# Performance work log

Hardware: AMD Instinct MI355X
Metric: run time of the kernel (lower is better)

Reference implementation:

```python
import jax, jax.numpy as jnp
import numpy as np

L, D, H, P = 4096, 512, 512, 16  # seq_len, feature_dim, attention_hidden_dim, padding_size


def setup_inputs() -> dict:
    key = jax.random.key(0)
    k1, k2, k3, k4 = jax.random.split(key, 4)
    x = jax.random.normal(k1, (L, D), dtype=jnp.float32)
    s = 1.0 / np.sqrt(D).astype(np.float32)
    Ww = jax.random.uniform(k2, (H, D), jnp.float32, -s, s)   # nn.Linear(D, H, bias=False).weight
    Wu = jax.random.uniform(k3, (H, D), jnp.float32, -s, s)
    sv = 1.0 / np.sqrt(H).astype(np.float32)
    Wv = jax.random.uniform(k4, (1, H), jnp.float32, -sv, sv)  # nn.Linear(H, 1, bias=False).weight
    return {"x": x, "Ww": Ww, "Wu": Wu, "Wv": Wv}


def _window_gather(x):
    # zero-pad P rows on each end of the sequence, then for each position i
    # gather the 2P neighbors (P left, P right), excluding the center.
    xp = jnp.pad(x, ((P, P), (0, 0)))
    off = jnp.concatenate([jnp.arange(P), jnp.arange(P + 1, 2 * P + 1)])  # [2P]
    idx = jnp.arange(x.shape[0])[:, None] + off[None, :]                  # [L, 2P]
    return xp[idx]                                                        # [L, 2P, D]


def reference(x, Ww, Wu, Wv):
    x_local = _window_gather(x)                                  # [L, 2P, D]
    wx = x @ Ww.T                                                # [L, H] (center, computed once vs torch repeat)
    ux = jnp.einsum('lwd,hd->lwh', x_local, Wu)                  # [L, 2P, H]
    energy = jnp.tanh(wx[:, None, :] + ux)                       # [L, 2P, H]
    scores = jnp.einsum('lwh,h->lw', energy, Wv[0])              # [L, 2P]
    attn = jax.nn.softmax(scores, axis=1)                        # softmax over window
    g = jnp.einsum('lw,lwd->ld', attn, x_local)                  # [L, D]
    return g
```

## Files before the change

### kernel.cpp

```cpp
#include <hip/hip_runtime.h>

#define L_SEQ 4096
#define D_DIM 512
#define H_DIM 512
#define P_PAD 16
#define LB 4
#define LOG2E2 2.885390081777927f
#define LOG2E  1.4426950408889634f

typedef __bf16 bf16x8 __attribute__((ext_vector_type(8)));
typedef float  f32x4  __attribute__((ext_vector_type(4)));

extern "C" __device__ float __ocml_native_exp2_f32(float);

__device__ __forceinline__ float exp2_fast(float x) {
#if __has_builtin(__builtin_amdgcn_exp2f)
    return __builtin_amdgcn_exp2f(x);
#else
    return __ocml_native_exp2_f32(x);
#endif
}

__device__ __forceinline__ ushort f2bf(float f) {
    unsigned u = __float_as_uint(f);
    return (ushort)((u + 0x7FFFu + ((u >> 16) & 1u)) >> 16);
}

__global__ __launch_bounds__(256) void convert_kernel(
    const float* __restrict__ x, const float* __restrict__ Ww,
    const float* __restrict__ Wu, ushort* __restrict__ xb,
    ushort* __restrict__ Wwb, ushort* __restrict__ Wub)
{
    int i = blockIdx.x * 256 + threadIdx.x;
    const float* src; ushort* dst; int off;
    if (i < 524288)      { src = x;  dst = xb;  off = i; }
    else if (i < 589824) { src = Ww; dst = Wwb; off = i - 524288; }
    else                 { src = Wu; dst = Wub; off = i - 589824; }
    float4 v = ((const float4*)src)[off];
    ushort4 o;
    o.x = f2bf(v.x); o.y = f2bf(v.y); o.z = f2bf(v.z); o.w = f2bf(v.w);
    ((ushort4*)dst)[off] = o;
}

__global__ __launch_bounds__(256, 2) void dual_gemm_mfma(
    const ushort* __restrict__ xb, const ushort* __restrict__ Wwb,
    const ushort* __restrict__ Wub, float* __restrict__ Ew, float* __restrict__ Eu)
{
    const ushort* Bm = blockIdx.z ? Wub : Wwb;
    float*       out = blockIdx.z ? Eu : Ew;
    const int m0 = blockIdx.x * 128;
    const int n0 = blockIdx.y * 64;

    __shared__ __align__(16) ushort As[2][128 * 64];
    __shared__ __align__(16) ushort Bs[2][64 * 64];

    const int tid  = threadIdx.x;
    const int wv   = tid >> 6;
    const int lane = tid & 63;
    const int wm   = (wv >> 1) * 64;
    const int wn   = (wv & 1) * 32;
    const int lr   = lane & 15;
    const int lg   = lane >> 4;
    const int rx   = lr & 7;

    f32x4 acc[4][2] = {};

    auto stage = [&](int t, int buf) {
        const int k0 = t * 64;
        #pragma unroll
        for (int i = 0; i < 4; ++i) {
            int c = i * 256 + tid;
            int row = c >> 3, q = c & 7;
            const ushort* src = xb + (size_t)(m0 + row) * D_DIM + k0 + ((q ^ (row & 7)) * 8);
            ushort* dst = &As[buf][(i * 256 + wv * 64) * 8];
            __builtin_amdgcn_global_load_lds(
                (const __attribute__((address_space(1))) void*)src,
                (__attribute__((address_space(3))) void*)dst, 16, 0, 0);
        }
        #pragma unroll
        for (int i = 0; i < 2; ++i) {
            int c = i * 256 + tid;
            int row = c >> 3, q = c & 7;
            const ushort* src = Bm + (size_t)(n0 + row) * D_DIM + k0 + ((q ^ (row & 7)) * 8);
            ushort* dst = &Bs[buf][(i * 256 + wv * 64) * 8];
            __builtin_amdgcn_global_load_lds(
                (const __attribute__((address_space(1))) void*)src,
                (__attribute__((address_space(3))) void*)dst, 16, 0, 0);
        }
    };

    auto compute = [&](int buf) {
        #pragma unroll
        for (int kk = 0; kk < 2; ++kk) {
            bf16x8 a[4], b[2];
            #pragma unroll
            for (int mi = 0; mi < 4; ++mi)
                a[mi] = *(const bf16x8*)&As[buf][(wm + mi * 16 + lr) * 64 +
                                                 (((kk * 4 + lg) ^ rx) * 8)];
            #pragma unroll
            for (int ni = 0; ni < 2; ++ni)
                b[ni] = *(const bf16x8*)&Bs[buf][(wn + ni * 16 + lr) * 64 +
                                                 (((kk * 4 + lg) ^ rx) * 8)];
            #pragma unroll
            for (int mi = 0; mi < 4; ++mi)
                #pragma unroll
                for (int ni = 0; ni < 2; ++ni)
                    acc[mi][ni] = __builtin_amdgcn_mfma_f32_16x16x32_bf16(
                        a[mi], b[ni], acc[mi][ni], 0, 0, 0);
        }
    };

    stage(0, 0);
    __syncthreads();
    #pragma unroll
    for (int t = 0; t < 7; ++t) {
        stage(t + 1, (t + 1) & 1);
        compute(t & 1);
        __syncthreads();
    }
    compute(1);

    #pragma unroll
    for (int mi = 0; mi < 4; ++mi)
        #pragma unroll
        for (int ni = 0; ni < 2; ++ni)
            #pragma unroll
            for (int r = 0; r < 4; ++r)
                out[(size_t)(m0 + wm + mi * 16 + lg * 4 + r) * H_DIM + n0 + wn + ni * 16 + lr] =
                    exp2_fast(LOG2E2 * acc[mi][ni][r]);
}

template<bool EDGE>
__device__ __forceinline__ float score_phase(
    const float* __restrict__ Eu, int l, int lane,
    const float* ewr, const float* wvn)
{
    const float* base = Eu + (size_t)l * H_DIM + lane * 8;
    float sc = 0.0f;
    #pragma unroll
    for (int wg = 0; wg < 8; ++wg) {
        f32x4 u[4][2];
        #pragma unroll
        for (int wi = 0; wi < 4; ++wi) {
            const int w = wg * 4 + wi;
            const int j = (w < P_PAD) ? (w - P_PAD) : (w - P_PAD + 1);
            const float* p;
            if (EDGE) {
                int n = l + j;
                n = min(max(n, 0), L_SEQ - 1);
                p = Eu + (size_t)n * H_DIM + lane * 8;
            } else {
                p = base + j * H_DIM;
            }
            u[wi][0] = ((const f32x4*)p)[0];
            u[wi][1] = ((const f32x4*)p)[1];
        }
        float a4[4];
        #pragma unroll
        for (int wi = 0; wi < 4; ++wi) {
            float a = 0.0f;
            #pragma unroll
            for (int e = 0; e < 8; ++e) {
                float eu = u[wi][e >> 2][e & 3];
                float q  = __builtin_fmaf(ewr[e], eu, 1.0f);
                a = __builtin_fmaf(wvn[e], __builtin_amdgcn_rcpf(q), a);
            }
            a4[wi] = a;
        }
        const bool b0 = lane & 1, b1 = lane & 2;
        float s01 = b0 ? a4[0] : a4[1];
        float r01 = __shfl_xor(s01, 1);
        float c0  = (b0 ? a4[1] : a4[0]) + r01;
        float s23 = b0 ? a4[2] : a4[3];
        float r23 = __shfl_xor(s23, 1);
        float c1  = (b0 ? a4[3] : a4[2]) + r23;
        float s2  = b1 ? c0 : c1;
        float r2  = __shfl_xor(s2, 2);
        float c   = (b1 ? c1 : c0) + r2;
        c += __shfl_xor(c, 4);
        c += __shfl_xor(c, 8);
        c += __shfl_xor(c, 16);
        c += __shfl_xor(c, 32);
        sc = ((lane >> 2) == wg) ? c : sc;
    }

    if (EDGE) {
        float a = 0.0f;
        #pragma unroll
        for (int e = 0; e < 8; ++e)
            a = __builtin_fmaf(wvn[e], __builtin_amdgcn_rcpf(ewr[e] + 1.0f), a);
        #pragma unroll
        for (int off = 32; off; off >>= 1) a += __shfl_xor(a, off);
        const int w = lane & 31;
        const int j = (w < P_PAD) ? (w - P_PAD) : (w - P_PAD + 1);
        const int n = l + j;
        if (n < 0 || n >= L_SEQ) sc = a;
    }
    return sc;
}

__global__ __launch_bounds__(256, 4) void attn_kernel(
    const float* __restrict__ x, const float* __restrict__ Ew,
    const float* __restrict__ Eu, const float* __restrict__ Wv,
    float* __restrict__ g)
{
    const int bid  = (blockIdx.x & 7) * 128 + (blockIdx.x >> 3);
    const int l0   = bid * LB;
    const int tid  = threadIdx.x;
    const int wave = tid >> 6;
    const int lane = tid & 63;
    const int l    = l0 + wave;

    __shared__ float sc_lds[LB][32];
    __shared__ float at_lds[LB][32];

    float ewr[8], wvn[8];
    {
        const f32x4* ewp = (const f32x4*)&Ew[(size_t)l * H_DIM + lane * 8];
        const f32x4* wvp = (const f32x4*)&Wv[lane * 8];
        f32x4 a0 = ewp[0], a1 = ewp[1], v0 = wvp[0], v1 = wvp[1];
        #pragma unroll
        for (int e = 0; e < 4; ++e) {
            ewr[e]     = a0[e];
            ewr[e + 4] = a1[e];
            wvn[e]     = -2.0f * v0[e];
            wvn[e + 4] = -2.0f * v1[e];
        }
    }

    float sc;
    if (l0 >= P_PAD && l0 + LB + P_PAD <= L_SEQ)
        sc = score_phase<false>(Eu, l, lane, ewr, wvn);
    else
        sc = score_phase<true>(Eu, l, lane, ewr, wvn);

    if (lane < 32) sc_lds[wave][lane] = sc;
    __syncthreads();

    if (tid < LB * 32) {
        const int ll = tid >> 5, w = tid & 31;
        float s0 = sc_lds[ll][w];
        float m = s0;
        #pragma unroll
        for (int off = 16; off; off >>= 1) m = fmaxf(m, __shfl_xor(m, off, 32));
        float e = exp2_fast((s0 - m) * LOG2E);
        float sum = e;
        #pragma unroll
        for (int off = 16; off; off >>= 1) sum += __shfl_xor(sum, off, 32);
        at_lds[ll][w] = e * __builtin_amdgcn_rcpf(sum);
    }
    __syncthreads();

    const int d = tid * 2;
    float2 acc[LB];
    #pragma unroll
    for (int li = 0; li < LB; ++li) acc[li] = make_float2(0.f, 0.f);

    #pragma unroll
    for (int t = 0; t < LB + 2 * P_PAD; ++t) {
        const int n = l0 - P_PAD + t;
        if (n >= 0 && n < L_SEQ) {
            float2 xv = *(const float2*)&x[(size_t)n * D_DIM + d];
            #pragma unroll
            for (int li = 0; li < LB; ++li) {
                const int j = t - P_PAD - li;
                if (j >= -P_PAD && j <= P_PAD && j != 0) {
                    const int w = (j < 0) ? j + P_PAD : j + P_PAD - 1;
                    float a = at_lds[li][w];
                    acc[li].x = __builtin_fmaf(a, xv.x, acc[li].x);
                    acc[li].y = __builtin_fmaf(a, xv.y, acc[li].y);
                }
            }
        }
    }
    #pragma unroll
    for (int li = 0; li < LB; ++li)
        *(float2*)&g[(size_t)(l0 + li) * D_DIM + d] = acc[li];
}

extern "C" void kernel_launch(void* const* d_in, const int* in_sizes, int n_in,
                              void* d_out, int out_size, void* d_ws, size_t ws_size,
                              hipStream_t stream) {
    const float* x  = (const float*)d_in[0];
    const float* Ww = (const float*)d_in[1];
    const float* Wu = (const float*)d_in[2];
    const float* Wv = (const float*)d_in[3];
    float* g = (float*)d_out;

    float*  Ew  = (float*)d_ws;
    float*  Eu  = Ew + (size_t)L_SEQ * H_DIM;
    ushort* xb  = (ushort*)(Eu + (size_t)L_SEQ * H_DIM);
    ushort* Wwb = xb + (size_t)L_SEQ * D_DIM;
    ushort* Wub = Wwb + (size_t)H_DIM * D_DIM;

    convert_kernel<<<dim3(2560), 256, 0, stream>>>(x, Ww, Wu, xb, Wwb, Wub);
    dual_gemm_mfma<<<dim3(L_SEQ / 128, H_DIM / 64, 2), 256, 0, stream>>>(xb, Wwb, Wub, Ew, Eu);
    attn_kernel<<<dim3(L_SEQ / LB), 256, 0, stream>>>(x, Ew, Eu, Wv, g);
}
```

Measured before the change: 45.79 us.

## Store exp intermediates in bf16 and split scoring into a separate kernel

```diff
diff --git a/kernel.cpp b/kernel.cpp
--- a/kernel.cpp
+++ b/kernel.cpp
@@ -10,6 +10,7 @@
 
 typedef __bf16 bf16x8 __attribute__((ext_vector_type(8)));
 typedef float  f32x4  __attribute__((ext_vector_type(4)));
+typedef unsigned short u16x8 __attribute__((ext_vector_type(8)));
 
 extern "C" __device__ float __ocml_native_exp2_f32(float);
 
@@ -24,6 +25,9 @@
 __device__ __forceinline__ ushort f2bf(float f) {
     unsigned u = __float_as_uint(f);
     return (ushort)((u + 0x7FFFu + ((u >> 16) & 1u)) >> 16);
+}
+__device__ __forceinline__ float bf2f(ushort s) {
+    return __uint_as_float((unsigned)s << 16);
 }
 
 __global__ __launch_bounds__(256) void convert_kernel(
@@ -44,10 +48,10 @@
 
 __global__ __launch_bounds__(256, 2) void dual_gemm_mfma(
     const ushort* __restrict__ xb, const ushort* __restrict__ Wwb,
-    const ushort* __restrict__ Wub, float* __restrict__ Ew, float* __restrict__ Eu)
+    const ushort* __restrict__ Wub, ushort* __restrict__ Ewb, ushort* __restrict__ Eub)
 {
     const ushort* Bm = blockIdx.z ? Wub : Wwb;
-    float*       out = blockIdx.z ? Eu : Ew;
+    ushort*      out = blockIdx.z ? Eub : Ewb;
     const int m0 = blockIdx.x * 128;
     const int n0 = blockIdx.y * 64;
 
@@ -127,119 +131,93 @@
             #pragma unroll
             for (int r = 0; r < 4; ++r)
                 out[(size_t)(m0 + wm + mi * 16 + lg * 4 + r) * H_DIM + n0 + wn + ni * 16 + lr] =
-                    exp2_fast(LOG2E2 * acc[mi][ni][r]);
-}
-
-template<bool EDGE>
-__device__ __forceinline__ float score_phase(
-    const float* __restrict__ Eu, int l, int lane,
-    const float* ewr, const float* wvn)
-{
-    const float* base = Eu + (size_t)l * H_DIM + lane * 8;
-    float sc = 0.0f;
-    #pragma unroll
-    for (int wg = 0; wg < 8; ++wg) {
-        f32x4 u[4][2];
-        #pragma unroll
-        for (int wi = 0; wi < 4; ++wi) {
-            const int w = wg * 4 + wi;
-            const int j = (w < P_PAD) ? (w - P_PAD) : (w - P_PAD + 1);
-            const float* p;
-            if (EDGE) {
-                int n = l + j;
-                n = min(max(n, 0), L_SEQ - 1);
-                p = Eu + (size_t)n * H_DIM + lane * 8;
-            } else {
-                p = base + j * H_DIM;
-            }
-            u[wi][0] = ((const f32x4*)p)[0];
-            u[wi][1] = ((const f32x4*)p)[1];
-        }
-        float a4[4];
-        #pragma unroll
-        for (int wi = 0; wi < 4; ++wi) {
-            float a = 0.0f;
-            #pragma unroll
-            for (int e = 0; e < 8; ++e) {
-                float eu = u[wi][e >> 2][e & 3];
-                float q  = __builtin_fmaf(ewr[e], eu, 1.0f);
-                a = __builtin_fmaf(wvn[e], __builtin_amdgcn_rcpf(q), a);
-            }
-            a4[wi] = a;
-        }
-        const bool b0 = lane & 1, b1 = lane & 2;
-        float s01 = b0 ? a4[0] : a4[1];
-        float r01 = __shfl_xor(s01, 1);
-        float c0  = (b0 ? a4[1] : a4[0]) + r01;
-        float s23 = b0 ? a4[2] : a4[3];
-        float r23 = __shfl_xor(s23, 1);
-        float c1  = (b0 ? a4[3] : a4[2]) + r23;
-        float s2  = b1 ? c0 : c1;
-        float r2  = __shfl_xor(s2, 2);
-        float c   = (b1 ? c1 : c0) + r2;
-        c += __shfl_xor(c, 4);
-        c += __shfl_xor(c, 8);
-        c += __shfl_xor(c, 16);
-        c += __shfl_xor(c, 32);
-        sc = ((lane >> 2) == wg) ? c : sc;
-    }
-
-    if (EDGE) {
+                    f2bf(exp2_fast(LOG2E2 * acc[mi][ni][r]));
+}
+
+__global__ __launch_bounds__(256, 6) void scores_kernel(
+    const ushort* __restrict__ Ewb, const ushort* __restrict__ Eub,
+    const float* __restrict__ Wv, float* __restrict__ scores)
+{
+    const int bid  = (blockIdx.x & 7) * 1024 + (blockIdx.x >> 3);
+    const int wave = threadIdx.x >> 6;
+    const int lane = threadIdx.x & 63;
+    const int task = bid * 4 + wave;
+    const int l    = task >> 3;
+    const int wg   = task & 7;
+
+    float ewr[8], wvn[8];
+    {
+        u16x8 ew8 = *(const u16x8*)&Ewb[(size_t)l * H_DIM + lane * 8];
+        const f32x4* wvp = (const f32x4*)&Wv[lane * 8];
+        f32x4 v0 = wvp[0], v1 = wvp[1];
+        #pragma unroll
+        for (int e = 0; e < 8; ++e) ewr[e] = bf2f(ew8[e]);
+        #pragma unroll
+        for (int e = 0; e < 4; ++e) { wvn[e] = -2.0f * v0[e]; wvn[e + 4] = -2.0f * v1[e]; }
+    }
+
+    float aoob = 0.0f;
+    if (l < P_PAD || l >= L_SEQ - P_PAD) {
+        #pragma unroll
+        for (int e = 0; e < 8; ++e)
+            aoob = __builtin_fmaf(wvn[e], __builtin_amdgcn_rcpf(ewr[e] + 1.0f), aoob);
+    }
+
+    u16x8 u[4];
+    int valid[4];
+    #pragma unroll
+    for (int wi = 0; wi < 4; ++wi) {
+        const int w = wg * 4 + wi;
+        const int j = (w < P_PAD) ? (w - P_PAD) : (w - P_PAD + 1);
+        int n = l + j;
+        valid[wi] = ((unsigned)n < (unsigned)L_SEQ);
+        n = min(max(n, 0), L_SEQ - 1);
+        u[wi] = *(const u16x8*)&Eub[(size_t)n * H_DIM + lane * 8];
+    }
+    float a4[4];
+    #pragma unroll
+    for (int wi = 0; wi < 4; ++wi) {
         float a = 0.0f;
         #pragma unroll
-        for (int e = 0; e < 8; ++e)
-            a = __builtin_fmaf(wvn[e], __builtin_amdgcn_rcpf(ewr[e] + 1.0f), a);
-        #pragma unroll
-        for (int off = 32; off; off >>= 1) a += __shfl_xor(a, off);
-        const int w = lane & 31;
-        const int j = (w < P_PAD) ? (w - P_PAD) : (w - P_PAD + 1);
-        const int n = l + j;
-        if (n < 0 || n >= L_SEQ) sc = a;
-    }
-    return sc;
-}
-
-__global__ __launch_bounds__(256, 4) void attn_kernel(
-    const float* __restrict__ x, const float* __restrict__ Ew,
-    const float* __restrict__ Eu, const float* __restrict__ Wv,
+        for (int e = 0; e < 8; ++e) {
+            float eu = bf2f(u[wi][e]);
+            float q  = __builtin_fmaf(ewr[e], eu, 1.0f);
+            a = __builtin_fmaf(wvn[e], __builtin_amdgcn_rcpf(q), a);
+        }
+        a4[wi] = valid[wi] ? a : aoob;
+    }
+
+    const bool b0 = lane & 1, b1 = lane & 2;
+    float s01 = b0 ? a4[0] : a4[1];
+    float r01 = __shfl_xor(s01, 1);
+    float c0  = (b0 ? a4[1] : a4[0]) + r01;
+    float s23 = b0 ? a4[2] : a4[3];
+    float r23 = __shfl_xor(s23, 1);
+    float c1  = (b0 ? a4[3] : a4[2]) + r23;
+    float s2  = b1 ? c0 : c1;
+    float r2  = __shfl_xor(s2, 2);
+    float c   = (b1 ? c1 : c0) + r2;
+    c += __shfl_xor(c, 4);
+    c += __shfl_xor(c, 8);
+    c += __shfl_xor(c, 16);
+    c += __shfl_xor(c, 32);
+
+    if (lane < 4) scores[l * 32 + wg * 4 + lane] = c;
+}
+
+__global__ __launch_bounds__(256, 8) void gather_kernel(
+    const float* __restrict__ x, const float* __restrict__ scores,
     float* __restrict__ g)
 {
     const int bid  = (blockIdx.x & 7) * 128 + (blockIdx.x >> 3);
     const int l0   = bid * LB;
     const int tid  = threadIdx.x;
-    const int wave = tid >> 6;
-    const int lane = tid & 63;
-    const int l    = l0 + wave;
-
-    __shared__ float sc_lds[LB][32];
+
     __shared__ float at_lds[LB][32];
-
-    float ewr[8], wvn[8];
-    {
-        const f32x4* ewp = (const f32x4*)&Ew[(size_t)l * H_DIM + lane * 8];
-        const f32x4* wvp = (const f32x4*)&Wv[lane * 8];
-        f32x4 a0 = ewp[0], a1 = ewp[1], v0 = wvp[0], v1 = wvp[1];
-        #pragma unroll
-        for (int e = 0; e < 4; ++e) {
-            ewr[e]     = a0[e];
-            ewr[e + 4] = a1[e];
-            wvn[e]     = -2.0f * v0[e];
-            wvn[e + 4] = -2.0f * v1[e];
-        }
-    }
-
-    float sc;
-    if (l0 >= P_PAD && l0 + LB + P_PAD <= L_SEQ)
-        sc = score_phase<false>(Eu, l, lane, ewr, wvn);
-    else
-        sc = score_phase<true>(Eu, l, lane, ewr, wvn);
-
-    if (lane < 32) sc_lds[wave][lane] = sc;
-    __syncthreads();
 
     if (tid < LB * 32) {
         const int ll = tid >> 5, w = tid & 31;
-        float s0 = sc_lds[ll][w];
+        float s0 = scores[(l0 + ll) * 32 + w];
         float m = s0;
         #pragma unroll
         for (int off = 16; off; off >>= 1) m = fmaxf(m, __shfl_xor(m, off, 32));
@@ -287,13 +265,15 @@
     const float* Wv = (const float*)d_in[3];
     float* g = (float*)d_out;
 
-    float*  Ew  = (float*)d_ws;
-    float*  Eu  = Ew + (size_t)L_SEQ * H_DIM;
-    ushort* xb  = (ushort*)(Eu + (size_t)L_SEQ * H_DIM);
+    ushort* Ewb = (ushort*)d_ws;
+    ushort* Eub = Ewb + (size_t)L_SEQ * H_DIM;
+    ushort* xb  = Eub + (size_t)L_SEQ * H_DIM;
     ushort* Wwb = xb + (size_t)L_SEQ * D_DIM;
     ushort* Wub = Wwb + (size_t)H_DIM * D_DIM;
+    float* scores = (float*)(Wub + (size_t)H_DIM * D_DIM);
 
     convert_kernel<<<dim3(2560), 256, 0, stream>>>(x, Ww, Wu, xb, Wwb, Wub);
-    dual_gemm_mfma<<<dim3(L_SEQ / 128, H_DIM / 64, 2), 256, 0, stream>>>(xb, Wwb, Wub, Ew, Eu);
-    attn_kernel<<<dim3(L_SEQ / LB), 256, 0, stream>>>(x, Ew, Eu, Wv, g);
-}
+    dual_gemm_mfma<<<dim3(L_SEQ / 128, H_DIM / 64, 2), 256, 0, stream>>>(xb, Wwb, Wub, Ewb, Eub);
+    scores_kernel<<<dim3(8192), 256, 0, stream>>>(Ewb, Eub, Wv, scores);
+    gather_kernel<<<dim3(L_SEQ / LB), 256, 0, stream>>>(x, scores, g);
+}
```

Result: slower. 47.03 us (+2.7%).
